# Performance work log

Measured on AMD Instinct MI355X. Metric: run time of the kernel, lower is better.

Reference implementation:

```python
import jax, jax.numpy as jnp
import numpy as np

K = 10          # hardcoded in module (self.K = 10)
H = 26          # neighbors per query point in this run
PAD_H = 28      # layer_ind2neighbor[layer_ind=0]
KP_EXTENT = 1.2 # linear-influence extent


def setup_inputs() -> dict:
    key = jax.random.key(0)
    ks = jax.random.split(key, 6)
    N, Ns, Cin, Cout = 65536, 65536, 64, 128
    q_pts = jax.random.normal(ks[0], (N, 3), jnp.float32)
    s_pts = jax.random.normal(ks[1], (Ns, 3), jnp.float32)
    neighb_inds = jax.random.randint(ks[2], (N, H), 0, Ns)
    x = jax.random.normal(ks[3], (Ns, Cin), jnp.float32)
    # kernel_points_generator: Linear(PAD_H*3 -> K*3)
    gen_W = jax.random.normal(ks[4], (K * 3, PAD_H * 3), jnp.float32) * (1.0 / np.sqrt(PAD_H * 3))
    gen_b = jnp.zeros((K * 3,), jnp.float32)
    # KPConv weights: [K, in, out] (kaiming_uniform in torch; scaled normal here)
    weights = jax.random.normal(ks[5], (K, Cin, Cout), jnp.float32) * (1.0 / np.sqrt(Cin))
    return {"q_pts": q_pts, "s_pts": s_pts, "x": x,
            "gen_W": gen_W, "gen_b": gen_b, "weights": weights,
            "neighb_inds": neighb_inds}


def _kpconv(q_pts, s_pts, x, gen_W, gen_b, weights, neighb_inds):
    N = q_pts.shape[0]
    # shadow support point far away (index Ns)
    s_pad = jnp.concatenate([s_pts, jnp.full((1, 3), 1e6, s_pts.dtype)], axis=0)
    neighbors = s_pad[neighb_inds] - q_pts[:, None, :]                          # [N,H,3]
    # generative kernel points: pad neighbor list with -1 up to PAD_H, run linear
    padded = jnp.concatenate(
        [neighbors, jnp.full((N, PAD_H - H, 3), -1.0, neighbors.dtype)], axis=1)
    kp = (padded.reshape(N, -1) @ gen_W.T + gen_b).reshape(N, 1, K, 3)          # [N,1,K,3]
    diff = neighbors[:, :, None, :] - kp                                        # [N,H,K,3]
    sq_d = jnp.sum(diff * diff, axis=3)                                         # [N,H,K]
    # KP_influence == 'linear'
    all_w = jnp.maximum(1.0 - jnp.sqrt(sq_d) / KP_EXTENT, 0.0)
    all_w = jnp.swapaxes(all_w, 1, 2)                                           # [N,K,H]
    # shadow feature row (zeros) at index Ns
    x_pad = jnp.concatenate([x, jnp.zeros((1, x.shape[1]), x.dtype)], axis=0)
    neighb_x = x_pad[neighb_inds]                                               # [N,H,Cin]
    weighted = jnp.einsum('nkh,nhi->nki', all_w, neighb_x)                      # [N,K,Cin]
    return jnp.einsum('nki,kio->no', weighted, weights)                         # [N,Cout]


def reference(q_pts, s_pts, x, gen_W, gen_b, weights, neighb_inds):
    return _kpconv(q_pts, s_pts, x, gen_W, gen_b, weights, neighb_inds)
```

## Files before the change

kernel.cpp:

```cpp
#include <hip/hip_runtime.h>
#include <stdint.h>

#define N_Q   65536
#define N_S   65536
#define NB_H  26
#define PAD_H 28
#define KP    10
#define CIN   64
#define COUT  128
#define MT    8
#define BM    64

typedef unsigned short u16x4  __attribute__((ext_vector_type(4)));
typedef unsigned short u16x8  __attribute__((ext_vector_type(8)));
typedef float          f32x4  __attribute__((ext_vector_type(4)));
typedef float          f32x2  __attribute__((ext_vector_type(2)));
typedef _Float16       f16x8  __attribute__((ext_vector_type(8)));
typedef _Float16       f16x2  __attribute__((ext_vector_type(2)));

#define CVT_BLOCKS 2049
#define PACK_BLOCKS 40

static __device__ __forceinline__ unsigned short f2h(float f) {
  return __builtin_bit_cast(unsigned short, (_Float16)f);
}

static __device__ __forceinline__ unsigned int pkrtz_u32(float a, float b) {
  return __builtin_bit_cast(unsigned int, __builtin_amdgcn_cvt_pkrtz(a, b));
}
static __device__ __forceinline__ float h2f_lo(unsigned int u) {
  return (float)__builtin_bit_cast(_Float16, (unsigned short)(u & 0xffffu));
}
static __device__ __forceinline__ float h2f_hi(unsigned int u) {
  return (float)__builtin_bit_cast(_Float16, (unsigned short)(u >> 16));
}

__global__ void prep_kernel(const float* __restrict__ x,
                            const float* __restrict__ w,
                            unsigned short* __restrict__ xh,
                            unsigned short* __restrict__ bp) {
  if (blockIdx.x < CVT_BLOCKS) {
    long t = (long)blockIdx.x * blockDim.x + threadIdx.x;
    long off = t * 8;
    if (off >= (long)(N_S + 1) * CIN) return;
    u16x8 o;
    if (off < (long)N_S * CIN) {
      f32x4 a = *(const f32x4*)(x + off);
      f32x4 b = *(const f32x4*)(x + off + 4);
      o[0] = f2h(a[0]); o[1] = f2h(a[1]); o[2] = f2h(a[2]); o[3] = f2h(a[3]);
      o[4] = f2h(b[0]); o[5] = f2h(b[1]); o[6] = f2h(b[2]); o[7] = f2h(b[3]);
    } else {
      o = (u16x8)0;
    }
    *(u16x8*)(xh + off) = o;
  } else {
    int t = (blockIdx.x - CVT_BLOCKS) * blockDim.x + threadIdx.x;
    if (t >= 8 * 20 * 64) return;
    int lane = t & 63;
    int frag = t >> 6;
    int ks = frag % 20;
    int ct = frag / 20;
    int row0 = ks * 32 + (lane >> 4) * 8;
    int col  = ct * 16 + (lane & 15);
    u16x8 o;
    #pragma unroll
    for (int j = 0; j < 8; ++j) o[j] = f2h(w[(row0 + j) * COUT + col]);
    *(u16x8*)(bp + (long)t * 8) = o;
  }
}

__global__ void __launch_bounds__(256, 8)
kpconv_gather(const float* __restrict__ q_pts, const float* __restrict__ s_pts,
              const float* __restrict__ gen_W, const float* __restrict__ gen_b,
              const int* __restrict__ inds, const unsigned short* __restrict__ xh,
              unsigned short* __restrict__ wg) {

  __shared__ int          sh_ind[MT][NB_H];
  __shared__ float        sh_nbr[MT][80];
  __shared__ float        sh_kp[MT][KP * 3];
  __shared__ int          sh_cnt[MT];
  __shared__ unsigned int sh_hoff[MT][NB_H];
  __shared__ float        sh_w[MT][NB_H][12];

  const int tid  = threadIdx.x;
  const int base = blockIdx.x * MT;

  if (tid < MT) sh_cnt[tid] = 0;
  if (tid < MT * NB_H) {
    int m = tid / NB_H, h = tid % NB_H;
    int n = base + m;
    int ind = inds[n * NB_H + h];
    sh_ind[m][h] = ind;
    float sx, sy, sz;
    if ((unsigned)ind < (unsigned)N_S) {
      sx = s_pts[ind * 3 + 0]; sy = s_pts[ind * 3 + 1]; sz = s_pts[ind * 3 + 2];
    } else {
      sx = 1e6f; sy = 1e6f; sz = 1e6f;
    }
    sh_nbr[m][h * 3 + 0] = sx - q_pts[n * 3 + 0];
    sh_nbr[m][h * 3 + 1] = sy - q_pts[n * 3 + 1];
    sh_nbr[m][h * 3 + 2] = sz - q_pts[n * 3 + 2];
  }
  if (tid < MT * 2) sh_nbr[tid >> 1][78 + (tid & 1)] = -1.0f;
  __syncthreads();

  if (tid < MT * KP * 3) {
    int m = tid / 30, r = tid % 30;
    const float* Wr = gen_W + r * (PAD_H * 3);
    const f32x4* W4 = (const f32x4*)Wr;
    const f32x4* N4 = (const f32x4*)&sh_nbr[m][0];
    f32x4 accv = {0.f, 0.f, 0.f, 0.f};
    #pragma unroll
    for (int j = 0; j < 20; ++j) accv += W4[j] * N4[j];
    sh_kp[m][r] = gen_b[r] - (Wr[80] + Wr[81] + Wr[82] + Wr[83])
                + accv[0] + accv[1] + accv[2] + accv[3];
  }
  __syncthreads();

  if (tid < MT * NB_H) {
    int m = tid / NB_H, h = tid % NB_H;
    float nx = sh_nbr[m][h * 3 + 0];
    float ny = sh_nbr[m][h * 3 + 1];
    float nz = sh_nbr[m][h * 3 + 2];
    float wv[KP];
    bool any = false;
    #pragma unroll
    for (int k = 0; k < KP; ++k) {
      float dx = nx - sh_kp[m][k * 3 + 0];
      float dy = ny - sh_kp[m][k * 3 + 1];
      float dz = nz - sh_kp[m][k * 3 + 2];
      float d  = sqrtf(dx * dx + dy * dy + dz * dz);
      float w  = fmaxf(1.0f - d * (1.0f / 1.2f), 0.0f);
      wv[k] = w;
      any = any || (w > 0.0f);
    }
    if (any) {
      int s = atomicAdd(&sh_cnt[m], 1);
      sh_hoff[m][s] = (unsigned int)sh_ind[m][h] * CIN;
      #pragma unroll
      for (int k = 0; k < KP; ++k) sh_w[m][s][k] = wv[k];
    }
  }
  __syncthreads();

  {
    const int m  = tid >> 5;
    const int i0 = (tid & 31) * 2;
    const int c  = sh_cnt[m];
    f32x2 acc[KP];
    #pragma unroll
    for (int k = 0; k < KP; ++k) acc[k] = (f32x2){0.f, 0.f};

    unsigned int xr0 = 0, xr1 = 0, xr2 = 0, xr3 = 0;
    if (0 < c) xr0 = *(const unsigned int*)(xh + sh_hoff[m][0] + i0);
    if (1 < c) xr1 = *(const unsigned int*)(xh + sh_hoff[m][1] + i0);
    if (2 < c) xr2 = *(const unsigned int*)(xh + sh_hoff[m][2] + i0);
    if (3 < c) xr3 = *(const unsigned int*)(xh + sh_hoff[m][3] + i0);

    #define C_BODY(J, XR)                                                     \
      {                                                                       \
        unsigned int cur = XR;                                                \
        if ((J) + 4 < c) XR = *(const unsigned int*)(xh + sh_hoff[m][(J) + 4] + i0); \
        f32x2 xp = { h2f_lo(cur), h2f_hi(cur) };                              \
        f32x4 wa = *(const f32x4*)&sh_w[m][J][0];                             \
        f32x4 wb = *(const f32x4*)&sh_w[m][J][4];                             \
        f32x2 wc = *(const f32x2*)&sh_w[m][J][8];                             \
        acc[0] += (f32x2){wa[0], wa[0]} * xp;                                 \
        acc[1] += (f32x2){wa[1], wa[1]} * xp;                                 \
        acc[2] += (f32x2){wa[2], wa[2]} * xp;                                 \
        acc[3] += (f32x2){wa[3], wa[3]} * xp;                                 \
        acc[4] += (f32x2){wb[0], wb[0]} * xp;                                 \
        acc[5] += (f32x2){wb[1], wb[1]} * xp;                                 \
        acc[6] += (f32x2){wb[2], wb[2]} * xp;                                 \
        acc[7] += (f32x2){wb[3], wb[3]} * xp;                                 \
        acc[8] += (f32x2){wc[0], wc[0]} * xp;                                 \
        acc[9] += (f32x2){wc[1], wc[1]} * xp;                                 \
      }

    for (int j0 = 0; j0 < c; j0 += 4) {
      C_BODY(j0, xr0);
      if (j0 + 1 < c) C_BODY(j0 + 1, xr1);
      if (j0 + 2 < c) C_BODY(j0 + 2, xr2);
      if (j0 + 3 < c) C_BODY(j0 + 3, xr3);
    }
    #undef C_BODY

    #pragma unroll
    for (int k = 0; k < KP; ++k) {
      __builtin_nontemporal_store(
          pkrtz_u32(acc[k][0], acc[k][1]),
          (unsigned int*)(wg + (long)(base + m) * (KP * CIN) + k * CIN + i0));
    }
  }
}

__global__ void __launch_bounds__(256, 4)
kpconv_gemm(const unsigned short* __restrict__ wg,
            const unsigned short* __restrict__ bp,
            float* __restrict__ out) {

  __shared__ unsigned short sA[2][BM][72];

  const int tid  = threadIdx.x;
  const int wave = tid >> 6;
  const int lane = tid & 63;
  const long row0 = (long)blockIdx.x * BM;

  const int srow = tid >> 3;
  const int scb  = tid & 7;

  {
    u16x8 a = __builtin_nontemporal_load((const u16x8*)(wg + (row0 + srow) * 640 + scb * 8));
    u16x8 b = __builtin_nontemporal_load((const u16x8*)(wg + (row0 + srow + 32) * 640 + scb * 8));
    *(u16x8*)&sA[0][srow][scb * 8] = a;
    *(u16x8*)&sA[0][srow + 32][scb * 8] = b;
  }

  f32x4 acc[4][2];
  #pragma unroll
  for (int rt = 0; rt < 4; ++rt)
    #pragma unroll
    for (int c = 0; c < 2; ++c) acc[rt][c] = (f32x4){0.f, 0.f, 0.f, 0.f};

  const int ct0  = wave * 2, ct1 = ct0 + 1;
  const int arow = lane & 15;
  const int aq   = lane >> 4;
  int cur = 0;

  for (int kc = 0; kc < 10; ++kc) {
    __syncthreads();
    u16x8 p0, p1;
    if (kc < 9) {
      p0 = __builtin_nontemporal_load((const u16x8*)(wg + (row0 + srow) * 640 + (kc + 1) * 64 + scb * 8));
      p1 = __builtin_nontemporal_load((const u16x8*)(wg + (row0 + srow + 32) * 640 + (kc + 1) * 64 + scb * 8));
    }
    #pragma unroll
    for (int ks2 = 0; ks2 < 2; ++ks2) {
      int ks = kc * 2 + ks2;
      u16x8 b0u = *(const u16x8*)(bp + (long)((ct0 * 20 + ks) * 64 + lane) * 8);
      u16x8 b1u = *(const u16x8*)(bp + (long)((ct1 * 20 + ks) * 64 + lane) * 8);
      f16x8 b0 = __builtin_bit_cast(f16x8, b0u);
      f16x8 b1 = __builtin_bit_cast(f16x8, b1u);
      #pragma unroll
      for (int rt = 0; rt < 4; ++rt) {
        u16x8 au = *(const u16x8*)&sA[cur][rt * 16 + arow][ks2 * 32 + aq * 8];
        f16x8 a = __builtin_bit_cast(f16x8, au);
        acc[rt][0] = __builtin_amdgcn_mfma_f32_16x16x32_f16(a, b0, acc[rt][0], 0, 0, 0);
        acc[rt][1] = __builtin_amdgcn_mfma_f32_16x16x32_f16(a, b1, acc[rt][1], 0, 0, 0);
      }
    }
    if (kc < 9) {
      *(u16x8*)&sA[1 - cur][srow][scb * 8] = p0;
      *(u16x8*)&sA[1 - cur][srow + 32][scb * 8] = p1;
      cur ^= 1;
    }
  }

  const int col   = lane & 15;
  const int rbase = aq * 4;
  #pragma unroll
  for (int rt = 0; rt < 4; ++rt)
    #pragma unroll
    for (int r = 0; r < 4; ++r) {
      long row = row0 + rt * 16 + rbase + r;
      __builtin_nontemporal_store(acc[rt][0][r], &out[row * COUT + ct0 * 16 + col]);
      __builtin_nontemporal_store(acc[rt][1][r], &out[row * COUT + ct1 * 16 + col]);
    }
}

extern "C" void kernel_launch(void* const* d_in, const int* in_sizes, int n_in,
                              void* d_out, int out_size, void* d_ws, size_t ws_size,
                              hipStream_t stream) {
  const float* q_pts = (const float*)d_in[0];
  const float* s_pts = (const float*)d_in[1];
  const float* x     = (const float*)d_in[2];
  const float* gen_W = (const float*)d_in[3];
  const float* gen_b = (const float*)d_in[4];
  const float* wts   = (const float*)d_in[5];
  const int*   inds  = (const int*)d_in[6];
  float* out = (float*)d_out;

  unsigned short* xh = (unsigned short*)d_ws;
  unsigned short* bp = xh + (size_t)(N_S + 1) * CIN;
  unsigned short* wg = bp + (size_t)81920;

  prep_kernel<<<CVT_BLOCKS + PACK_BLOCKS, 256, 0, stream>>>(x, wts, xh, bp);
  kpconv_gather<<<N_Q / MT, 256, 0, stream>>>(q_pts, s_pts, gen_W, gen_b,
                                              inds, xh, wg);
  kpconv_gemm<<<N_Q / BM, 256, 0, stream>>>(wg, bp, out);
}
```

Before: 176.8 us.

## Fuse gather and GEMM into one kernel, gather fp32 x directly

Merges the gather/weighting kernel and the MFMA GEMM kernel into a single kernel. Each block handles 16 query points and keeps the [16,640] fp16 intermediate in LDS instead of writing it to global memory and reading it back. It also drops the fp16 conversion pass over x and gathers fp32 rows directly, which doubles the bytes per gathered row but removes a full read and write of x. The GEMM stage is now 16-row tiles with one 16x16 MFMA tile per wave, giving less reuse of B and larger blocks with more LDS.

```diff
diff --git a/kernel.cpp b/kernel.cpp
--- a/kernel.cpp
+++ b/kernel.cpp
@@ -8,79 +8,51 @@
 #define KP    10
 #define CIN   64
 #define COUT  128
-#define MT    8
-#define BM    64
-
-typedef unsigned short u16x4  __attribute__((ext_vector_type(4)));
+#define MT    16
+
 typedef unsigned short u16x8  __attribute__((ext_vector_type(8)));
 typedef float          f32x4  __attribute__((ext_vector_type(4)));
 typedef float          f32x2  __attribute__((ext_vector_type(2)));
 typedef _Float16       f16x8  __attribute__((ext_vector_type(8)));
-typedef _Float16       f16x2  __attribute__((ext_vector_type(2)));
-
-#define CVT_BLOCKS 2049
-#define PACK_BLOCKS 40
 
 static __device__ __forceinline__ unsigned short f2h(float f) {
   return __builtin_bit_cast(unsigned short, (_Float16)f);
 }
-
 static __device__ __forceinline__ unsigned int pkrtz_u32(float a, float b) {
   return __builtin_bit_cast(unsigned int, __builtin_amdgcn_cvt_pkrtz(a, b));
 }
-static __device__ __forceinline__ float h2f_lo(unsigned int u) {
-  return (float)__builtin_bit_cast(_Float16, (unsigned short)(u & 0xffffu));
-}
-static __device__ __forceinline__ float h2f_hi(unsigned int u) {
-  return (float)__builtin_bit_cast(_Float16, (unsigned short)(u >> 16));
-}
-
-__global__ void prep_kernel(const float* __restrict__ x,
-                            const float* __restrict__ w,
-                            unsigned short* __restrict__ xh,
+
+__global__ void prep_kernel(const float* __restrict__ w,
                             unsigned short* __restrict__ bp) {
-  if (blockIdx.x < CVT_BLOCKS) {
-    long t = (long)blockIdx.x * blockDim.x + threadIdx.x;
-    long off = t * 8;
-    if (off >= (long)(N_S + 1) * CIN) return;
-    u16x8 o;
-    if (off < (long)N_S * CIN) {
-      f32x4 a = *(const f32x4*)(x + off);
-      f32x4 b = *(const f32x4*)(x + off + 4);
-      o[0] = f2h(a[0]); o[1] = f2h(a[1]); o[2] = f2h(a[2]); o[3] = f2h(a[3]);
-      o[4] = f2h(b[0]); o[5] = f2h(b[1]); o[6] = f2h(b[2]); o[7] = f2h(b[3]);
-    } else {
-      o = (u16x8)0;
-    }
-    *(u16x8*)(xh + off) = o;
-  } else {
-    int t = (blockIdx.x - CVT_BLOCKS) * blockDim.x + threadIdx.x;
-    if (t >= 8 * 20 * 64) return;
-    int lane = t & 63;
-    int frag = t >> 6;
-    int ks = frag % 20;
-    int ct = frag / 20;
-    int row0 = ks * 32 + (lane >> 4) * 8;
-    int col  = ct * 16 + (lane & 15);
-    u16x8 o;
-    #pragma unroll
-    for (int j = 0; j < 8; ++j) o[j] = f2h(w[(row0 + j) * COUT + col]);
-    *(u16x8*)(bp + (long)t * 8) = o;
-  }
-}
-
-__global__ void __launch_bounds__(256, 8)
-kpconv_gather(const float* __restrict__ q_pts, const float* __restrict__ s_pts,
-              const float* __restrict__ gen_W, const float* __restrict__ gen_b,
-              const int* __restrict__ inds, const unsigned short* __restrict__ xh,
-              unsigned short* __restrict__ wg) {
+  int t = blockIdx.x * blockDim.x + threadIdx.x;
+  if (t >= 8 * 20 * 64) return;
+  int lane = t & 63;
+  int frag = t >> 6;
+  int ks = frag % 20;
+  int ct = frag / 20;
+  int row0 = ks * 32 + (lane >> 4) * 8;
+  int col  = ct * 16 + (lane & 15);
+  u16x8 o;
+  #pragma unroll
+  for (int j = 0; j < 8; ++j) o[j] = f2h(w[(row0 + j) * COUT + col]);
+  *(u16x8*)(bp + (long)t * 8) = o;
+}
+
+__global__ void __launch_bounds__(512, 6)
+kpconv_fused(const float* __restrict__ q_pts, const float* __restrict__ s_pts,
+             const float* __restrict__ x, const float* __restrict__ gen_W,
+             const float* __restrict__ gen_b, const int* __restrict__ inds,
+             const unsigned short* __restrict__ bp, float* __restrict__ out) {
 
   __shared__ int          sh_ind[MT][NB_H];
-  __shared__ float        sh_nbr[MT][80];
-  __shared__ float        sh_kp[MT][KP * 3];
+  __shared__ unsigned int sh_hoff[MT][NB_H];
   __shared__ int          sh_cnt[MT];
-  __shared__ unsigned int sh_hoff[MT][NB_H];
-  __shared__ float        sh_w[MT][NB_H][12];
+  __shared__ __align__(16) char pool[27008];
+
+  float* sh_nbr = (float*)pool;
+  float* sh_kp  = (float*)(pool + 5120);
+  float* sh_w   = (float*)(pool + 7040);
+  unsigned short* sh_frag = (unsigned short*)pool;
 
   const int tid  = threadIdx.x;
   const int base = blockIdx.x * MT;
@@ -97,38 +69,38 @@
     } else {
       sx = 1e6f; sy = 1e6f; sz = 1e6f;
     }
-    sh_nbr[m][h * 3 + 0] = sx - q_pts[n * 3 + 0];
-    sh_nbr[m][h * 3 + 1] = sy - q_pts[n * 3 + 1];
-    sh_nbr[m][h * 3 + 2] = sz - q_pts[n * 3 + 2];
-  }
-  if (tid < MT * 2) sh_nbr[tid >> 1][78 + (tid & 1)] = -1.0f;
+    sh_nbr[m * 80 + h * 3 + 0] = sx - q_pts[n * 3 + 0];
+    sh_nbr[m * 80 + h * 3 + 1] = sy - q_pts[n * 3 + 1];
+    sh_nbr[m * 80 + h * 3 + 2] = sz - q_pts[n * 3 + 2];
+  }
+  if (tid < MT * 2) sh_nbr[(tid >> 1) * 80 + 78 + (tid & 1)] = -1.0f;
   __syncthreads();
 
   if (tid < MT * KP * 3) {
     int m = tid / 30, r = tid % 30;
     const float* Wr = gen_W + r * (PAD_H * 3);
     const f32x4* W4 = (const f32x4*)Wr;
-    const f32x4* N4 = (const f32x4*)&sh_nbr[m][0];
+    const f32x4* N4 = (const f32x4*)&sh_nbr[m * 80];
     f32x4 accv = {0.f, 0.f, 0.f, 0.f};
     #pragma unroll
     for (int j = 0; j < 20; ++j) accv += W4[j] * N4[j];
-    sh_kp[m][r] = gen_b[r] - (Wr[80] + Wr[81] + Wr[82] + Wr[83])
-                + accv[0] + accv[1] + accv[2] + accv[3];
+    sh_kp[m * 30 + r] = gen_b[r] - (Wr[80] + Wr[81] + Wr[82] + Wr[83])
+                      + accv[0] + accv[1] + accv[2] + accv[3];
   }
   __syncthreads();
 
   if (tid < MT * NB_H) {
     int m = tid / NB_H, h = tid % NB_H;
-    float nx = sh_nbr[m][h * 3 + 0];
-    float ny = sh_nbr[m][h * 3 + 1];
-    float nz = sh_nbr[m][h * 3 + 2];
+    float nx = sh_nbr[m * 80 + h * 3 + 0];
+    float ny = sh_nbr[m * 80 + h * 3 + 1];
+    float nz = sh_nbr[m * 80 + h * 3 + 2];
     float wv[KP];
     bool any = false;
     #pragma unroll
     for (int k = 0; k < KP; ++k) {
-      float dx = nx - sh_kp[m][k * 3 + 0];
-      float dy = ny - sh_kp[m][k * 3 + 1];
-      float dz = nz - sh_kp[m][k * 3 + 2];
+      float dx = nx - sh_kp[m * 30 + k * 3 + 0];
+      float dy = ny - sh_kp[m * 30 + k * 3 + 1];
+      float dz = nz - sh_kp[m * 30 + k * 3 + 2];
       float d  = sqrtf(dx * dx + dy * dy + dz * dz);
       float w  = fmaxf(1.0f - d * (1.0f / 1.2f), 0.0f);
       wv[k] = w;
@@ -138,7 +110,7 @@
       int s = atomicAdd(&sh_cnt[m], 1);
       sh_hoff[m][s] = (unsigned int)sh_ind[m][h] * CIN;
       #pragma unroll
-      for (int k = 0; k < KP; ++k) sh_w[m][s][k] = wv[k];
+      for (int k = 0; k < KP; ++k) sh_w[m * 312 + s * 12 + k] = wv[k];
     }
   }
   __syncthreads();
@@ -151,20 +123,20 @@
     #pragma unroll
     for (int k = 0; k < KP; ++k) acc[k] = (f32x2){0.f, 0.f};
 
-    unsigned int xr0 = 0, xr1 = 0, xr2 = 0, xr3 = 0;
-    if (0 < c) xr0 = *(const unsigned int*)(xh + sh_hoff[m][0] + i0);
-    if (1 < c) xr1 = *(const unsigned int*)(xh + sh_hoff[m][1] + i0);
-    if (2 < c) xr2 = *(const unsigned int*)(xh + sh_hoff[m][2] + i0);
-    if (3 < c) xr3 = *(const unsigned int*)(xh + sh_hoff[m][3] + i0);
+    f32x2 xr0 = {0.f,0.f}, xr1 = {0.f,0.f}, xr2 = {0.f,0.f}, xr3 = {0.f,0.f};
+    if (0 < c) xr0 = *(const f32x2*)(x + sh_hoff[m][0] + i0);
+    if (1 < c) xr1 = *(const f32x2*)(x + sh_hoff[m][1] + i0);
+    if (2 < c) xr2 = *(const f32x2*)(x + sh_hoff[m][2] + i0);
+    if (3 < c) xr3 = *(const f32x2*)(x + sh_hoff[m][3] + i0);
 
     #define C_BODY(J, XR)                                                     \
       {                                                                       \
-        unsigned int cur = XR;                                                \
-        if ((J) + 4 < c) XR = *(const unsigned int*)(xh + sh_hoff[m][(J) + 4] + i0); \
-        f32x2 xp = { h2f_lo(cur), h2f_hi(cur) };                              \
-        f32x4 wa = *(const f32x4*)&sh_w[m][J][0];                             \
-        f32x4 wb = *(const f32x4*)&sh_w[m][J][4];                             \
-        f32x2 wc = *(const f32x2*)&sh_w[m][J][8];                             \
+        f32x2 xp = XR;                                                        \
+        if ((J) + 4 < c) XR = *(const f32x2*)(x + sh_hoff[m][(J) + 4] + i0);  \
+        const float* wr = &sh_w[m * 312 + (J) * 12];                          \
+        f32x4 wa = *(const f32x4*)&wr[0];                                     \
+        f32x4 wb = *(const f32x4*)&wr[4];                                     \
+        f32x2 wc = *(const f32x2*)&wr[8];                                     \
         acc[0] += (f32x2){wa[0], wa[0]} * xp;                                 \
         acc[1] += (f32x2){wa[1], wa[1]} * xp;                                 \
         acc[2] += (f32x2){wa[2], wa[2]} * xp;                                 \
@@ -185,87 +157,35 @@
     }
     #undef C_BODY
 
+    __syncthreads();
     #pragma unroll
     for (int k = 0; k < KP; ++k) {
+      *(unsigned int*)&sh_frag[m * 648 + k * CIN + i0] = pkrtz_u32(acc[k][0], acc[k][1]);
+    }
+  }
+  __syncthreads();
+
+  {
+    const int ct   = tid >> 6;
+    const int lane = tid & 63;
+    const int arow = lane & 15;
+    const int ak   = (lane >> 4) * 8;
+    f32x4 acc = {0.f, 0.f, 0.f, 0.f};
+    for (int ks = 0; ks < 20; ++ks) {
+      u16x8 au = *(const u16x8*)&sh_frag[arow * 648 + ks * 32 + ak];
+      u16x8 bu = *(const u16x8*)(bp + (long)((ct * 20 + ks) * 64 + lane) * 8);
+      f16x8 a = __builtin_bit_cast(f16x8, au);
+      f16x8 b = __builtin_bit_cast(f16x8, bu);
+      acc = __builtin_amdgcn_mfma_f32_16x16x32_f16(a, b, acc, 0, 0, 0);
+    }
+    const int col   = lane & 15;
+    const int rbase = (lane >> 4) * 4;
+    #pragma unroll
+    for (int r = 0; r < 4; ++r) {
       __builtin_nontemporal_store(
-          pkrtz_u32(acc[k][0], acc[k][1]),
-          (unsigned int*)(wg + (long)(base + m) * (KP * CIN) + k * CIN + i0));
-    }
-  }
-}
-
-__global__ void __launch_bounds__(256, 4)
-kpconv_gemm(const unsigned short* __restrict__ wg,
-            const unsigned short* __restrict__ bp,
-            float* __restrict__ out) {
-
-  __shared__ unsigned short sA[2][BM][72];
-
-  const int tid  = threadIdx.x;
-  const int wave = tid >> 6;
-  const int lane = tid & 63;
-  const long row0 = (long)blockIdx.x * BM;
-
-  const int srow = tid >> 3;
-  const int scb  = tid & 7;
-
-  {
-    u16x8 a = __builtin_nontemporal_load((const u16x8*)(wg + (row0 + srow) * 640 + scb * 8));
-    u16x8 b = __builtin_nontemporal_load((const u16x8*)(wg + (row0 + srow + 32) * 640 + scb * 8));
-    *(u16x8*)&sA[0][srow][scb * 8] = a;
-    *(u16x8*)&sA[0][srow + 32][scb * 8] = b;
-  }
-
-  f32x4 acc[4][2];
-  #pragma unroll
-  for (int rt = 0; rt < 4; ++rt)
-    #pragma unroll
-    for (int c = 0; c < 2; ++c) acc[rt][c] = (f32x4){0.f, 0.f, 0.f, 0.f};
-
-  const int ct0  = wave * 2, ct1 = ct0 + 1;
-  const int arow = lane & 15;
-  const int aq   = lane >> 4;
-  int cur = 0;
-
-  for (int kc = 0; kc < 10; ++kc) {
-    __syncthreads();
-    u16x8 p0, p1;
-    if (kc < 9) {
-      p0 = __builtin_nontemporal_load((const u16x8*)(wg + (row0 + srow) * 640 + (kc + 1) * 64 + scb * 8));
-      p1 = __builtin_nontemporal_load((const u16x8*)(wg + (row0 + srow + 32) * 640 + (kc + 1) * 64 + scb * 8));
-    }
-    #pragma unroll
-    for (int ks2 = 0; ks2 < 2; ++ks2) {
-      int ks = kc * 2 + ks2;
-      u16x8 b0u = *(const u16x8*)(bp + (long)((ct0 * 20 + ks) * 64 + lane) * 8);
-      u16x8 b1u = *(const u16x8*)(bp + (long)((ct1 * 20 + ks) * 64 + lane) * 8);
-      f16x8 b0 = __builtin_bit_cast(f16x8, b0u);
-      f16x8 b1 = __builtin_bit_cast(f16x8, b1u);
-      #pragma unroll
-      for (int rt = 0; rt < 4; ++rt) {
-        u16x8 au = *(const u16x8*)&sA[cur][rt * 16 + arow][ks2 * 32 + aq * 8];
-        f16x8 a = __builtin_bit_cast(f16x8, au);
-        acc[rt][0] = __builtin_amdgcn_mfma_f32_16x16x32_f16(a, b0, acc[rt][0], 0, 0, 0);
-        acc[rt][1] = __builtin_amdgcn_mfma_f32_16x16x32_f16(a, b1, acc[rt][1], 0, 0, 0);
-      }
-    }
-    if (kc < 9) {
-      *(u16x8*)&sA[1 - cur][srow][scb * 8] = p0;
-      *(u16x8*)&sA[1 - cur][srow + 32][scb * 8] = p1;
-      cur ^= 1;
-    }
-  }
-
-  const int col   = lane & 15;
-  const int rbase = aq * 4;
-  #pragma unroll
-  for (int rt = 0; rt < 4; ++rt)
-    #pragma unroll
-    for (int r = 0; r < 4; ++r) {
-      long row = row0 + rt * 16 + rbase + r;
-      __builtin_nontemporal_store(acc[rt][0][r], &out[row * COUT + ct0 * 16 + col]);
-      __builtin_nontemporal_store(acc[rt][1][r], &out[row * COUT + ct1 * 16 + col]);
-    }
+          acc[r], &out[(long)(base + rbase + r) * COUT + ct * 16 + col]);
+    }
+  }
 }
 
 extern "C" void kernel_launch(void* const* d_in, const int* in_sizes, int n_in,
@@ -280,12 +200,9 @@
   const int*   inds  = (const int*)d_in[6];
   float* out = (float*)d_out;
 
-  unsigned short* xh = (unsigned short*)d_ws;
-  unsigned short* bp = xh + (size_t)(N_S + 1) * CIN;
-  unsigned short* wg = bp + (size_t)81920;
-
-  prep_kernel<<<CVT_BLOCKS + PACK_BLOCKS, 256, 0, stream>>>(x, wts, xh, bp);
-  kpconv_gather<<<N_Q / MT, 256, 0, stream>>>(q_pts, s_pts, gen_W, gen_b,
-                                              inds, xh, wg);
-  kpconv_gemm<<<N_Q / BM, 256, 0, stream>>>(wg, bp, out);
-}
+  unsigned short* bp = (unsigned short*)d_ws;
+
+  prep_kernel<<<40, 256, 0, stream>>>(wts, bp);
+  kpconv_fused<<<N_Q / MT, 512, 0, stream>>>(q_pts, s_pts, x, gen_W, gen_b,
+                                             inds, bp, out);
+}
```

Measured after the change: 176.9 us. Within noise of the previous version (+0.0%).
